# Kernel optimization log

Hardware: AMD Instinct MI355X
Metric: run time of the kernel (lower is better)

## Reference

```python
import jax, jax.numpy as jnp
import numpy as np

B, NUM_PEAKS, PEAK_SIZE = 2, 64, 1000
MOTIF, HID, DEPTH, PROF_K = 640, 256, 7, 75


def conv1d(x, w, b, dilation=1):
    # x: (N, C, L), w: (O, I, K), valid padding
    out = jax.lax.conv_general_dilated(
        x, w, window_strides=(1,), padding='VALID',
        rhs_dilation=(dilation,), dimension_numbers=('NCH', 'OIH', 'NCH'))
    return out + b[None, :, None]


def setup_inputs() -> dict:
    key = jax.random.key(0)
    ks = jax.random.split(key, 10)
    L = NUM_PEAKS * PEAK_SIZE
    x = jax.random.normal(ks[0], (B, L, MOTIF), dtype=jnp.float32)
    peak_split = jnp.full((B * NUM_PEAKS,), PEAK_SIZE, dtype=jnp.int64) if jax.config.jax_enable_x64 else jnp.full((B * NUM_PEAKS,), PEAK_SIZE, dtype=jnp.int32)
    n_peaks = jnp.full((B,), NUM_PEAKS, dtype=jnp.int32)
    # parameters (kaiming-ish small init)
    w_proj = jax.random.normal(ks[1], (HID, MOTIF, 1), dtype=jnp.float32) / np.sqrt(MOTIF)
    b_proj = jnp.zeros((HID,), jnp.float32)
    w_dil = jax.random.normal(ks[2], (DEPTH, HID, HID, 3), dtype=jnp.float32) / np.sqrt(3 * HID)
    b_dil = jnp.zeros((DEPTH, HID), jnp.float32)
    w_prof = jax.random.normal(ks[3], (1, HID, PROF_K), dtype=jnp.float32) / np.sqrt(PROF_K * HID)
    b_prof = jnp.zeros((1,), jnp.float32)
    w_atpm = jax.random.normal(ks[4], (1, HID), dtype=jnp.float32) / np.sqrt(HID)
    b_atpm = jnp.zeros((1,), jnp.float32)
    return {
        'x': x, 'peak_split': peak_split, 'n_peaks': n_peaks, 'max_n_peaks': NUM_PEAKS,
        'w_proj': w_proj, 'b_proj': b_proj, 'w_dil': w_dil, 'b_dil': b_dil,
        'w_prof': w_prof, 'b_prof': b_prof, 'w_atpm': w_atpm, 'b_atpm': b_atpm,
    }


def reference(x, peak_split, n_peaks, max_n_peaks,
              w_proj, b_proj, w_dil, b_dil, w_prof, b_prof, w_atpm, b_atpm):
    # fast path: all samples have max_n_peaks uniform-size peaks
    batch, length, _ = x.shape
    num_peaks = int(np.asarray(n_peaks)[0])
    peak_size = length // num_peaks
    # 1x1 motif projection: (B, L, MOTIF) -> (B, HID, L)
    h = conv1d(jnp.transpose(x, (0, 2, 1)), w_proj, b_proj)
    # split into peaks: (B*num_peaks, HID, peak_size)
    h = jnp.transpose(h, (0, 2, 1)).reshape(batch * num_peaks, peak_size, HID)
    h = jnp.transpose(h, (0, 2, 1))
    # dilated conv tower with residual crop
    for i in range(DEPTH):
        dilation = 2 ** (i + 1)
        out = conv1d(h, w_dil[i], b_dil[i], dilation=dilation)
        crop = (h.shape[-1] - out.shape[-1]) // 2
        h = jax.nn.relu(out) + h[..., crop:-crop]
    peak_atpm = h.mean(axis=2)                      # (N, HID)
    peak_profile = conv1d(h, w_prof, b_prof)        # (N, 1, out_len)
    peak_atpm = jax.nn.softplus(peak_atpm @ w_atpm.T + b_atpm)
    peak_atpm = peak_atpm.reshape(batch, num_peaks, 1)
    peak_profile = jax.nn.softplus(peak_profile.reshape(batch, -1))
    return (peak_atpm, peak_profile)
```

## Files before the change

kernel.cpp:

```cpp
#include <hip/hip_runtime.h>
#include <hip/hip_bf16.h>
#include <math.h>

#define HID 256
#define MOTIF 640
#define PEAK 1000
#define NPEAKS 128
#define DEPTHN 7
#define PROFK 75
#define FINLEN 492
#define PROFLEN 418

typedef unsigned short u16;
typedef unsigned int u32;
typedef _Float16 f16x8 __attribute__((ext_vector_type(8)));
typedef float f32x16 __attribute__((ext_vector_type(16)));

__device__ __forceinline__ u16 f2h(float f) {
    _Float16 h = (_Float16)f; u16 b; __builtin_memcpy(&b, &h, 2); return b;
}
__device__ __forceinline__ float h2f(u16 b) {
    _Float16 h; __builtin_memcpy(&h, &b, 2); return (float)h;
}
__device__ __forceinline__ float hlo(u32 u) { return h2f((u16)(u & 0xffff)); }
__device__ __forceinline__ float hhi(u32 u) { return h2f((u16)(u >> 16)); }
__device__ __forceinline__ u32 pk2h(float a, float b) {
    return (u32)f2h(a) | ((u32)f2h(b) << 16);
}

__device__ __forceinline__ void gll16(const void* g, void* l) {
    __builtin_amdgcn_global_load_lds(
        (const __attribute__((address_space(1))) void*)g,
        (__attribute__((address_space(3))) void*)l, 16, 0, 0);
}

__global__ __launch_bounds__(256) void conv_wdil_all(const float* __restrict__ w,
                                                     u16* __restrict__ wf,
                                                     float* __restrict__ zp) {
    const int layer = blockIdx.y;
    int i = blockIdx.x * 256 + threadIdx.x;
    if (layer == 0 && i < NPEAKS) zp[i] = 0.f;
    const float* wl = w + (size_t)layer * HID * HID * 3;
    u16* wfl = wf + (size_t)layer * (3 * HID * HID);
    int cil = i & 15; int j = i >> 4;
    int c = j & 255; j >>= 8;
    int ci16 = j & 15; int k = j >> 4;
    wfl[i] = f2h(wl[((size_t)c * HID + ci16 * 16 + cil) * 3 + k]);
}

__global__ __launch_bounds__(256) void conv_wproj(const float* __restrict__ w,
                                                  u16* __restrict__ wf) {
    int i = blockIdx.x * 256 + threadIdx.x;
    if (i >= MOTIF * HID) return;
    int ml = i & 15;
    int c = (i >> 4) & 255;
    int m16 = i >> 12;
    wf[i] = f2h(w[(size_t)c * MOTIF + m16 * 16 + ml]);
}

template<int NWC, int NWT, int TAPS, int KCI, int CCI, int DIL,
         bool SRCF32, bool RESID, bool ATPM>
__global__ __launch_bounds__(NWC * NWT * 64, (NWC * NWT == 8) ? 4 : 3)
void mfma_gemm(
    const void* __restrict__ src, int in_len, int in_stride,
    const u16* __restrict__ wf, const float* __restrict__ bias,
    u16* __restrict__ dst, int out_len,
    const float* __restrict__ watpm, float* part)
{
    constexpr int BS   = NWC * NWT * 64;
    constexpr int CW   = NWC * 64;
    constexpr int TW   = NWT * 64;
    constexpr int R    = TW + (TAPS - 1) * DIL;
    constexpr int GR   = CCI / 8;
    constexpr int SUBS = CCI / 16;
    constexpr int KTC  = TAPS * SUBS;
    constexpr int NC   = KCI / CCI;
    constexpr int ASLOTS = KTC * CW * 2;
    constexpr int AIT  = (ASLOTS + BS - 1) / BS;
    constexpr int BSLOTS = R * GR;
    constexpr int BIT  = (BSLOTS + BS - 1) / BS;
    constexpr int NIF  = SRCF32 ? AIT : (AIT + BIT);

    __shared__ __attribute__((aligned(16))) u16 As[2][(ASLOTS + 64) * 8];
    __shared__ __attribute__((aligned(16))) u16 Bs[2][(BSLOTS + 64) * 8];
    __shared__ float aw[NWC * NWT];
    const int tid = threadIdx.x;
    const int wave = tid >> 6, lane = tid & 63;
    const int col = lane & 31, half = lane >> 5;
    const int cg = wave % NWC, tg = wave / NWC;
    const int t0 = blockIdx.x * TW;
    const int c0 = blockIdx.y * CW;
    const int n  = blockIdx.z;

    const float* snf = (const float*)src + (size_t)n * in_len * in_stride;
    const u16*   snh = (const u16*)src + (size_t)n * in_len * in_stride;

    f32x16 acc[2][2];
    #pragma unroll
    for (int cs = 0; cs < 2; ++cs)
        #pragma unroll
        for (int ts = 0; ts < 2; ++ts)
            #pragma unroll
            for (int q = 0; q < 16; ++q) acc[cs][ts][q] = 0.f;

    auto stageA = [&](int cc, int b) {
        const int kt0 = (cc * CCI) >> 4;
        #pragma unroll
        for (int it = 0; it < AIT; ++it) {
            int s = it * BS + tid;
            if (s >= ASLOTS) s = ASLOTS - 1;
            const int ktl = s / (CW * 2);
            const int rem = s % (CW * 2);
            const int c = rem >> 1, hf = rem & 1;
            const int k = ktl / SUBS, sub = ktl % SUBS;
            const int ktg = k * (KCI / 16) + kt0 + sub;
            gll16(wf + (size_t)(ktg * 256 + c0 + c) * 16 + hf * 8,
                  &As[b][(size_t)s * 8]);
        }
    };
    auto stageB = [&](int cc, int b) {
        const int ci0 = cc * CCI;
        #pragma unroll
        for (int it = 0; it < BIT; ++it) {
            int s = it * BS + tid;
            if (s >= BSLOTS) s = BSLOTS - 1;
            const int r = s / GR, ch = s % GR;
            int g = t0 + r; if (g > in_len - 1) g = in_len - 1;
            const int chs = ch ^ (r & (GR - 1));
            if (SRCF32) {
                const float* p = snf + (size_t)g * in_stride + ci0 + chs * 8;
                float4 a = *(const float4*)p;
                float4 bq = *(const float4*)(p + 4);
                uint4 o;
                o.x = pk2h(a.x, a.y); o.y = pk2h(a.z, a.w);
                o.z = pk2h(bq.x, bq.y); o.w = pk2h(bq.z, bq.w);
                *(uint4*)&Bs[b][(size_t)s * 8] = o;
            } else {
                gll16(snh + (size_t)g * in_stride + ci0 + chs * 8,
                      &Bs[b][(size_t)s * 8]);
            }
        }
    };
    auto compute = [&](int b) {
        #pragma unroll
        for (int k = 0; k < TAPS; ++k) {
            #pragma unroll
            for (int sub = 0; sub < SUBS; ++sub) {
                const int ktl = k * SUBS + sub;
                f16x8 bf[2];
                #pragma unroll
                for (int ts = 0; ts < 2; ++ts) {
                    const int row = tg * 64 + ts * 32 + col + k * DIL;
                    const int sl = row * GR + ((sub * 2 + half) ^ (row & (GR - 1)));
                    bf[ts] = *reinterpret_cast<const f16x8*>(&Bs[b][(size_t)sl * 8]);
                }
                #pragma unroll
                for (int cs = 0; cs < 2; ++cs) {
                    const f16x8 af = *reinterpret_cast<const f16x8*>(
                        &As[b][(size_t)(ktl * (CW * 2) + (cg * 64 + cs * 32 + col) * 2 + half) * 8]);
                    acc[cs][0] = __builtin_amdgcn_mfma_f32_32x32x16_f16(af, bf[0], acc[cs][0], 0, 0, 0);
                    acc[cs][1] = __builtin_amdgcn_mfma_f32_32x32x16_f16(af, bf[1], acc[cs][1], 0, 0, 0);
                }
            }
        }
    };

    if (SRCF32) { stageB(0, 0); stageA(0, 0); stageB(1, 1); stageA(1, 1); }
    else        { stageA(0, 0); stageB(0, 0); stageA(1, 1); stageB(1, 1); }

    #pragma unroll
    for (int c = 0; c < NC; ++c) {
        if (SRCF32) asm volatile("s_waitcnt lgkmcnt(0)" ::: "memory");
        if (c + 1 < NC) asm volatile("s_waitcnt vmcnt(%0)" :: "i"(NIF) : "memory");
        else            asm volatile("s_waitcnt vmcnt(0)" ::: "memory");
        __builtin_amdgcn_s_barrier();
        asm volatile("" ::: "memory");
        compute(c & 1);
        asm volatile("" ::: "memory");
        __builtin_amdgcn_s_barrier();
        asm volatile("" ::: "memory");
        if (c + 2 < NC) {
            if (SRCF32) { stageB(c + 2, c & 1); stageA(c + 2, c & 1); }
            else        { stageA(c + 2, c & 1); stageB(c + 2, c & 1); }
        }
    }

    float apart = 0.f;
    #pragma unroll
    for (int ts = 0; ts < 2; ++ts) {
        const int t = t0 + tg * 64 + ts * 32 + col;
        if (t >= out_len) continue;
        const float* resf = snf + (size_t)(t + DIL) * in_stride;
        const u16*   resh = snh + (size_t)(t + DIL) * in_stride;
        u16* oh = dst + ((size_t)n * out_len + t) * HID;
        #pragma unroll
        for (int cs = 0; cs < 2; ++cs) {
            #pragma unroll
            for (int g = 0; g < 4; ++g) {
                const int c = c0 + cg * 64 + cs * 32 + g * 8 + half * 4;
                float4 bv = *(const float4*)(bias + c);
                float v0 = acc[cs][ts][g * 4 + 0] + bv.x;
                float v1 = acc[cs][ts][g * 4 + 1] + bv.y;
                float v2 = acc[cs][ts][g * 4 + 2] + bv.z;
                float v3 = acc[cs][ts][g * 4 + 3] + bv.w;
                if (RESID) {
                    if (SRCF32) {
                        float4 r = *(const float4*)(resf + c);
                        v0 = fmaxf(v0, 0.f) + r.x;
                        v1 = fmaxf(v1, 0.f) + r.y;
                        v2 = fmaxf(v2, 0.f) + r.z;
                        v3 = fmaxf(v3, 0.f) + r.w;
                    } else {
                        uint2 r = *(const uint2*)(resh + c);
                        v0 = fmaxf(v0, 0.f) + hlo(r.x);
                        v1 = fmaxf(v1, 0.f) + hhi(r.x);
                        v2 = fmaxf(v2, 0.f) + hlo(r.y);
                        v3 = fmaxf(v3, 0.f) + hhi(r.y);
                    }
                }
                if (ATPM) {
                    float4 wv = *(const float4*)(watpm + c);
                    apart += v0 * wv.x + v1 * wv.y + v2 * wv.z + v3 * wv.w;
                }
                uint2 o; o.x = pk2h(v0, v1); o.y = pk2h(v2, v3);
                *(uint2*)(oh + c) = o;
            }
        }
    }
    if (ATPM) {
        #pragma unroll
        for (int off = 32; off; off >>= 1) apart += __shfl_down(apart, off, 64);
        if (lane == 0) aw[wave] = apart;
        __syncthreads();
        if (tid == 0) {
            float s = 0.f;
            #pragma unroll
            for (int wv = 0; wv < NWC * NWT; ++wv) s += aw[wv];
            atomicAdd(part + n, s);
        }
    }
}

__global__ void atpm_fin(const float* __restrict__ part,
                         const float* __restrict__ batpm, float* __restrict__ out) {
    int i = threadIdx.x;
    float tot = part[i] / (float)FINLEN + batpm[0];
    out[i] = fmaxf(tot, 0.f) + log1pf(expf(-fabsf(tot)));
}

__global__ __launch_bounds__(256) void prof_kernel(
    const u16* __restrict__ h, const float* __restrict__ wprof,
    const float* __restrict__ bprof, float* __restrict__ out)
{
    __shared__ __attribute__((aligned(16))) float hs[64 * 204];
    __shared__ float red[128 * 8];
    const int tid = threadIdx.x;
    const int wave = tid >> 6, lane = tid & 63;
    const int ts = lane & 31, hw = lane >> 5;
    const int cig = wave * 2 + hw;
    const int n = blockIdx.y, t0 = blockIdx.x * 128;
    const u16* hn = h + (size_t)n * FINLEN * HID;
    float acc[4] = {0.f, 0.f, 0.f, 0.f};

    for (int ci0 = 0; ci0 < HID; ci0 += 64) {
        __syncthreads();
        {
            const int ci = tid & 63, rg = tid >> 6;
            for (int base = 0; base < 204; base += 16) {
                const int r0 = base + rg * 4;
                if (r0 >= 204) continue;
                float4 v;
                float* vp = (float*)&v;
                #pragma unroll
                for (int j = 0; j < 4; ++j) {
                    int g = t0 + r0 + j; if (g > FINLEN - 1) g = FINLEN - 1;
                    vp[j] = h2f(hn[(size_t)g * HID + ci0 + ci]);
                }
                *(float4*)&hs[ci * 204 + r0] = v;
            }
        }
        __syncthreads();
        for (int ci = 0; ci < 8; ++ci) {
            const int cia = cig * 8 + ci;
            const float4* hrow = (const float4*)&hs[cia * 204];
            const float* wrow = wprof + (size_t)(ci0 + cia) * PROFK;
            float wqf[84];
            #pragma unroll
            for (int q = 0; q < 3; ++q) wqf[q] = 0.f;
            #pragma unroll
            for (int q = 78; q < 84; ++q) wqf[q] = 0.f;
            #pragma unroll
            for (int k = 0; k < PROFK; ++k) wqf[k + 3] = wrow[k];
            #pragma unroll
            for (int m = 0; m < 20; ++m) {
                float4 h4 = hrow[ts + m];
                const float* hp = (const float*)&h4;
                #pragma unroll
                for (int j = 0; j < 4; ++j) {
                    #pragma unroll
                    for (int a = 0; a < 4; ++a) {
                        acc[a] += wqf[4 * m + j - a + 3] * hp[j];
                    }
                }
            }
        }
    }
    #pragma unroll
    for (int a = 0; a < 4; ++a) red[(ts * 4 + a) * 8 + cig] = acc[a];
    __syncthreads();
    if (tid < 128) {
        float s = 0.f;
        #pragma unroll
        for (int c8 = 0; c8 < 8; ++c8) s += red[tid * 8 + c8];
        const int t = t0 + tid;
        if (t < PROFLEN) {
            float v = s + bprof[0];
            out[(size_t)n * PROFLEN + t] = fmaxf(v, 0.f) + log1pf(expf(-fabsf(v)));
        }
    }
}

extern "C" void kernel_launch(void* const* d_in, const int* in_sizes, int n_in,
                              void* d_out, int out_size, void* d_ws, size_t ws_size,
                              hipStream_t stream) {
    const float* x     = (const float*)d_in[0];
    const float* wproj = (const float*)d_in[4];
    const float* bproj = (const float*)d_in[5];
    const float* wdil  = (const float*)d_in[6];
    const float* bdil  = (const float*)d_in[7];
    const float* wprof = (const float*)d_in[8];
    const float* bprof = (const float*)d_in[9];
    const float* watpm = (const float*)d_in[10];
    const float* batpm = (const float*)d_in[11];
    float* outAtpm = (float*)d_out;
    float* outProf = outAtpm + NPEAKS;

    char* ws = (char*)d_ws;
    u16* hA    = (u16*)ws;
    u16* hB    = (u16*)(ws + 65536000);
    u16* wpf   = (u16*)(ws + 131072000);
    u16* wslot = (u16*)(ws + 131399680);
    float* part = (float*)(ws + 134152192);

    conv_wproj<<<(MOTIF * HID + 255) / 256, 256, 0, stream>>>(wproj, wpf);
    conv_wdil_all<<<dim3(768, DEPTHN), 256, 0, stream>>>(wdil, wslot, part);

    mfma_gemm<4, 2, 1, MOTIF, 32, 0, true, false, false>
        <<<dim3(8, 1, NPEAKS), 512, 0, stream>>>(
        x, PEAK, MOTIF, wpf, bproj, hA, PEAK, nullptr, nullptr);

    #define LAYER(i, DIL, SRC, DST, INL, OUTL, TT)                                 \
        mfma_gemm<2, 4, 3, HID, 16, DIL, false, true, false>                       \
            <<<dim3(TT, 2, NPEAKS), 512, 0, stream>>>(                             \
            SRC, INL, HID, wslot + (size_t)(i) * (3 * HID * HID),                  \
            bdil + (size_t)(i) * HID, DST, OUTL, nullptr, nullptr);
    LAYER(0,   2, hA, hB, 1000, 996, 4)
    LAYER(1,   4, hB, hA,  996, 988, 4)
    LAYER(2,   8, hA, hB,  988, 972, 4)
    LAYER(3,  16, hB, hA,  972, 940, 4)
    LAYER(4,  32, hA, hB,  940, 876, 4)
    #undef LAYER
    mfma_gemm<2, 2, 3, HID, 16, 64, false, true, false>
        <<<dim3(6, 2, NPEAKS), 256, 0, stream>>>(
        hB, 876, HID, wslot + (size_t)5 * (3 * HID * HID), bdil + (size_t)5 * HID,
        hA, 748, nullptr, nullptr);
    mfma_gemm<2, 2, 3, HID, 16, 128, false, true, true>
        <<<dim3(4, 2, NPEAKS), 256, 0, stream>>>(
        hA, 748, HID, wslot + (size_t)6 * (3 * HID * HID), bdil + (size_t)6 * HID,
        hB, 492, watpm, part);

    atpm_fin<<<1, 128, 0, stream>>>(part, batpm, outAtpm);
    prof_kernel<<<dim3(4, NPEAKS), 256, 0, stream>>>(hB, wprof, bprof, outProf);
}
```

Before: 1.181 ms.

## Stage epilogue through LDS for coalesced stores and use uniform 256-thread tiles

Changes the shared-memory layouts of the A and B tiles from row-interleaved with an XOR swizzle to a plain channel-group-major order. Stages the accumulators through a swizzled LDS transpose buffer so each thread writes contiguous channel vectors per time row, which coalesces the residual loads and output stores. All tower layers and the projection now use 2x2-wave 256-thread blocks with twice as many time tiles, and launch bounds are fixed at 3. The cost is extra LDS use and barriers in the epilogue, a possible loss of bank-conflict protection in the unswizzled B layout, and lower occupancy for the larger configs.

Result: slower. 1.209 ms (+2.4%).

```diff
diff --git a/kernel.cpp b/kernel.cpp
--- a/kernel.cpp
+++ b/kernel.cpp
@@ -60,7 +60,7 @@
 
 template<int NWC, int NWT, int TAPS, int KCI, int CCI, int DIL,
          bool SRCF32, bool RESID, bool ATPM>
-__global__ __launch_bounds__(NWC * NWT * 64, (NWC * NWT == 8) ? 4 : 3)
+__global__ __launch_bounds__(NWC * NWT * 64, 3)
 void mfma_gemm(
     const void* __restrict__ src, int in_len, int in_stride,
     const u16* __restrict__ wf, const float* __restrict__ bias,
@@ -83,6 +83,7 @@
 
     __shared__ __attribute__((aligned(16))) u16 As[2][(ASLOTS + 64) * 8];
     __shared__ __attribute__((aligned(16))) u16 Bs[2][(BSLOTS + 64) * 8];
+    __shared__ __attribute__((aligned(16))) float Ct[32 * 128];
     __shared__ float aw[NWC * NWT];
     const int tid = threadIdx.x;
     const int wave = tid >> 6, lane = tid & 63;
@@ -111,7 +112,8 @@
             if (s >= ASLOTS) s = ASLOTS - 1;
             const int ktl = s / (CW * 2);
             const int rem = s % (CW * 2);
-            const int c = rem >> 1, hf = rem & 1;
+            const int hf = rem / CW;
+            const int c  = rem % CW;
             const int k = ktl / SUBS, sub = ktl % SUBS;
             const int ktg = k * (KCI / 16) + kt0 + sub;
             gll16(wf + (size_t)(ktg * 256 + c0 + c) * 16 + hf * 8,
@@ -124,11 +126,10 @@
         for (int it = 0; it < BIT; ++it) {
             int s = it * BS + tid;
             if (s >= BSLOTS) s = BSLOTS - 1;
-            const int r = s / GR, ch = s % GR;
+            const int gch = s / R, r = s % R;
             int g = t0 + r; if (g > in_len - 1) g = in_len - 1;
-            const int chs = ch ^ (r & (GR - 1));
             if (SRCF32) {
-                const float* p = snf + (size_t)g * in_stride + ci0 + chs * 8;
+                const float* p = snf + (size_t)g * in_stride + ci0 + gch * 8;
                 float4 a = *(const float4*)p;
                 float4 bq = *(const float4*)(p + 4);
                 uint4 o;
@@ -136,7 +137,7 @@
                 o.z = pk2h(bq.x, bq.y); o.w = pk2h(bq.z, bq.w);
                 *(uint4*)&Bs[b][(size_t)s * 8] = o;
             } else {
-                gll16(snh + (size_t)g * in_stride + ci0 + chs * 8,
+                gll16(snh + (size_t)g * in_stride + ci0 + gch * 8,
                       &Bs[b][(size_t)s * 8]);
             }
         }
@@ -151,13 +152,14 @@
                 #pragma unroll
                 for (int ts = 0; ts < 2; ++ts) {
                     const int row = tg * 64 + ts * 32 + col + k * DIL;
-                    const int sl = row * GR + ((sub * 2 + half) ^ (row & (GR - 1)));
-                    bf[ts] = *reinterpret_cast<const f16x8*>(&Bs[b][(size_t)sl * 8]);
+                    bf[ts] = *reinterpret_cast<const f16x8*>(
+                        &Bs[b][(size_t)((sub * 2 + half) * R + row) * 8]);
                 }
                 #pragma unroll
                 for (int cs = 0; cs < 2; ++cs) {
                     const f16x8 af = *reinterpret_cast<const f16x8*>(
-                        &As[b][(size_t)(ktl * (CW * 2) + (cg * 64 + cs * 32 + col) * 2 + half) * 8]);
+                        &As[b][(size_t)(ktl * (CW * 2) + half * CW
+                                        + cg * 64 + cs * 32 + col) * 8]);
                     acc[cs][0] = __builtin_amdgcn_mfma_f32_32x32x16_f16(af, bf[0], acc[cs][0], 0, 0, 0);
                     acc[cs][1] = __builtin_amdgcn_mfma_f32_32x32x16_f16(af, bf[1], acc[cs][1], 0, 0, 0);
                 }
@@ -186,44 +188,53 @@
     }
 
     float apart = 0.f;
+    const float4 bv = *(const float4*)(bias + c0 + col * 4);
+    float4 wv = {0.f, 0.f, 0.f, 0.f};
+    if (ATPM) wv = *(const float4*)(watpm + c0 + col * 4);
+
     #pragma unroll
-    for (int ts = 0; ts < 2; ++ts) {
-        const int t = t0 + tg * 64 + ts * 32 + col;
-        if (t >= out_len) continue;
-        const float* resf = snf + (size_t)(t + DIL) * in_stride;
-        const u16*   resh = snh + (size_t)(t + DIL) * in_stride;
-        u16* oh = dst + ((size_t)n * out_len + t) * HID;
-        #pragma unroll
-        for (int cs = 0; cs < 2; ++cs) {
-            #pragma unroll
-            for (int g = 0; g < 4; ++g) {
-                const int c = c0 + cg * 64 + cs * 32 + g * 8 + half * 4;
-                float4 bv = *(const float4*)(bias + c);
-                float v0 = acc[cs][ts][g * 4 + 0] + bv.x;
-                float v1 = acc[cs][ts][g * 4 + 1] + bv.y;
-                float v2 = acc[cs][ts][g * 4 + 2] + bv.z;
-                float v3 = acc[cs][ts][g * 4 + 3] + bv.w;
+    for (int p = 0; p < 4; ++p) {
+        __syncthreads();
+        if (tg == (p >> 1)) {
+            const int ts2 = p & 1;
+            #pragma unroll
+            for (int cs = 0; cs < 2; ++cs)
+                #pragma unroll
+                for (int g = 0; g < 4; ++g) {
+                    const int tl = col;
+                    const int cb = (cg * 64 + cs * 32 + g * 8 + half * 4) * 4;
+                    float4 o;
+                    o.x = acc[cs][ts2][g * 4 + 0];
+                    o.y = acc[cs][ts2][g * 4 + 1];
+                    o.z = acc[cs][ts2][g * 4 + 2];
+                    o.w = acc[cs][ts2][g * 4 + 3];
+                    *(float4*)((char*)Ct + tl * 512 + (cb ^ ((tl & 7) << 4))) = o;
+                }
+        }
+        __syncthreads();
+        #pragma unroll
+        for (int it2 = 0; it2 < 4; ++it2) {
+            const int tl = wave * 8 + it2 * 2 + half;
+            const int t = t0 + p * 32 + tl;
+            if (t < out_len) {
+                float4 v4 = *(const float4*)((const char*)Ct + tl * 512
+                                             + ((col * 16) ^ ((tl & 7) << 4)));
+                float v0 = v4.x + bv.x, v1 = v4.y + bv.y;
+                float v2 = v4.z + bv.z, v3 = v4.w + bv.w;
                 if (RESID) {
                     if (SRCF32) {
-                        float4 r = *(const float4*)(resf + c);
-                        v0 = fmaxf(v0, 0.f) + r.x;
-                        v1 = fmaxf(v1, 0.f) + r.y;
-                        v2 = fmaxf(v2, 0.f) + r.z;
-                        v3 = fmaxf(v3, 0.f) + r.w;
+                        float4 r = *(const float4*)(snf + (size_t)(t + DIL) * in_stride + c0 + col * 4);
+                        v0 = fmaxf(v0, 0.f) + r.x; v1 = fmaxf(v1, 0.f) + r.y;
+                        v2 = fmaxf(v2, 0.f) + r.z; v3 = fmaxf(v3, 0.f) + r.w;
                     } else {
-                        uint2 r = *(const uint2*)(resh + c);
-                        v0 = fmaxf(v0, 0.f) + hlo(r.x);
-                        v1 = fmaxf(v1, 0.f) + hhi(r.x);
-                        v2 = fmaxf(v2, 0.f) + hlo(r.y);
-                        v3 = fmaxf(v3, 0.f) + hhi(r.y);
+                        uint2 r = *(const uint2*)(snh + (size_t)(t + DIL) * in_stride + c0 + col * 4);
+                        v0 = fmaxf(v0, 0.f) + hlo(r.x); v1 = fmaxf(v1, 0.f) + hhi(r.x);
+                        v2 = fmaxf(v2, 0.f) + hlo(r.y); v3 = fmaxf(v3, 0.f) + hhi(r.y);
                     }
                 }
-                if (ATPM) {
-                    float4 wv = *(const float4*)(watpm + c);
-                    apart += v0 * wv.x + v1 * wv.y + v2 * wv.z + v3 * wv.w;
-                }
+                if (ATPM) apart += v0 * wv.x + v1 * wv.y + v2 * wv.z + v3 * wv.w;
                 uint2 o; o.x = pk2h(v0, v1); o.y = pk2h(v2, v3);
-                *(uint2*)(oh + c) = o;
+                *(uint2*)(dst + ((size_t)n * out_len + t) * HID + c0 + col * 4) = o;
             }
         }
     }
@@ -235,7 +246,7 @@
         if (tid == 0) {
             float s = 0.f;
             #pragma unroll
-            for (int wv = 0; wv < NWC * NWT; ++wv) s += aw[wv];
+            for (int wv2 = 0; wv2 < NWC * NWT; ++wv2) s += aw[wv2];
             atomicAdd(part + n, s);
         }
     }
@@ -345,25 +356,22 @@
     conv_wproj<<<(MOTIF * HID + 255) / 256, 256, 0, stream>>>(wproj, wpf);
     conv_wdil_all<<<dim3(768, DEPTHN), 256, 0, stream>>>(wdil, wslot, part);
 
-    mfma_gemm<4, 2, 1, MOTIF, 32, 0, true, false, false>
-        <<<dim3(8, 1, NPEAKS), 512, 0, stream>>>(
+    mfma_gemm<2, 2, 1, MOTIF, 32, 0, true, false, false>
+        <<<dim3(8, 2, NPEAKS), 256, 0, stream>>>(
         x, PEAK, MOTIF, wpf, bproj, hA, PEAK, nullptr, nullptr);
 
     #define LAYER(i, DIL, SRC, DST, INL, OUTL, TT)                                 \
-        mfma_gemm<2, 4, 3, HID, 16, DIL, false, true, false>                       \
-            <<<dim3(TT, 2, NPEAKS), 512, 0, stream>>>(                             \
+        mfma_gemm<2, 2, 3, HID, 16, DIL, false, true, false>                       \
+            <<<dim3(TT, 2, NPEAKS), 256, 0, stream>>>(                             \
             SRC, INL, HID, wslot + (size_t)(i) * (3 * HID * HID),                  \
             bdil + (size_t)(i) * HID, DST, OUTL, nullptr, nullptr);
-    LAYER(0,   2, hA, hB, 1000, 996, 4)
-    LAYER(1,   4, hB, hA,  996, 988, 4)
-    LAYER(2,   8, hA, hB,  988, 972, 4)
-    LAYER(3,  16, hB, hA,  972, 940, 4)
-    LAYER(4,  32, hA, hB,  940, 876, 4)
+    LAYER(0,   2, hA, hB, 1000, 996, 8)
+    LAYER(1,   4, hB, hA,  996, 988, 8)
+    LAYER(2,   8, hA, hB,  988, 972, 8)
+    LAYER(3,  16, hB, hA,  972, 940, 8)
+    LAYER(4,  32, hA, hB,  940, 876, 7)
+    LAYER(5,  64, hB, hA,  876, 748, 6)
     #undef LAYER
-    mfma_gemm<2, 2, 3, HID, 16, 64, false, true, false>
-        <<<dim3(6, 2, NPEAKS), 256, 0, stream>>>(
-        hB, 876, HID, wslot + (size_t)5 * (3 * HID * HID), bdil + (size_t)5 * HID,
-        hA, 748, nullptr, nullptr);
     mfma_gemm<2, 2, 3, HID, 16, 128, false, true, true>
         <<<dim3(4, 2, NPEAKS), 256, 0, stream>>>(
         hA, 748, HID, wslot + (size_t)6 * (3 * HID * HID), bdil + (size_t)6 * HID,
```
